# Kernel optimization log

Measured on AMD Instinct MI355X. Metric: run time of the kernel, lower is better.

Reference implementation:

```python
import jax, jax.numpy as jnp
import numpy as np

T = 16384
D_IN = 512
D_HID = 512
D_OUT = 512


def setup_inputs() -> dict:
    key = jax.random.key(0)
    ks = jax.random.split(key, 7)
    s_in = 1.0 / np.sqrt(D_IN)
    s_hid = 1.0 / np.sqrt(D_HID)
    xs = jax.random.normal(ks[0], (T, D_IN), dtype=jnp.float32)
    Wz = jax.random.uniform(ks[1], (D_HID, D_IN), jnp.float32, -s_in, s_in)
    bz = jax.random.uniform(ks[2], (D_HID,), jnp.float32, -s_in, s_in)
    Wh = jax.random.uniform(ks[3], (D_HID, D_IN), jnp.float32, -s_in, s_in)
    bh = jax.random.uniform(ks[4], (D_HID,), jnp.float32, -s_in, s_in)
    Wo = jax.random.uniform(ks[5], (D_OUT, D_HID), jnp.float32, -s_hid, s_hid)
    bo = jax.random.uniform(ks[6], (D_OUT,), jnp.float32, -s_hid, s_hid)
    return {"xs": xs, "Wz": Wz, "bz": bz, "Wh": Wh, "bh": bh, "Wo": Wo, "bo": bo}


def _combine(first, second):
    a0, b0 = first
    a1, b1 = second
    return (a0 * a1, a1 * b0 + b1)


def reference(xs, Wz, bz, Wh, bh, Wo, bo):
    # gates and candidate hidden states: [T, H]
    zs = jax.nn.sigmoid(xs @ Wz.T + bz)
    hs = xs @ Wh.T + bh
    # prepend identity element (a=1, b=0) for the h_0 = 0 initial state
    a = jnp.concatenate([jnp.ones((1, zs.shape[1]), zs.dtype), 1.0 - zs], axis=0)
    b = jnp.concatenate([jnp.zeros((1, zs.shape[1]), zs.dtype), zs * hs], axis=0)
    _, states = jax.lax.associative_scan(_combine, (a, b))  # [T+1, H]
    return states[1:] @ Wo.T + bo  # [T, D_OUT]
```

## Files before the change

kernel.cpp:

```cpp
#include <hip/hip_runtime.h>
#include <hip/hip_bf16.h>
#include <cstdint>
#include <cmath>

#define T_SEQ 16384
#define DMODEL 512
#define NCHUNK 512
#define LCHUNK 32
#define XS_N   (T_SEQ * DMODEL)
#define W_N    (DMODEL * DMODEL)
#define N4_XS  (XS_N / 4)
#define N4_W   (W_N / 4)
#define N4_TOT (N4_XS + 3 * N4_W)

typedef __bf16 bf16x8 __attribute__((ext_vector_type(8)));
typedef float  f32x4  __attribute__((ext_vector_type(4)));

using bf16 = __hip_bfloat16;

__device__ __forceinline__ void load_lds16(const void* g, void* l) {
    __builtin_amdgcn_global_load_lds((const __attribute__((address_space(1))) void*)g,
                                     (__attribute__((address_space(3))) void*)l,
                                     16, 0, 0);
}

__device__ __forceinline__ unsigned short f2bf(float f) {
    union { float f; unsigned u; } v; v.f = f;
    const unsigned r = (v.u + 0x7FFFu + ((v.u >> 16) & 1u)) >> 16;
    return (unsigned short)r;
}
__device__ __forceinline__ float bf2f(unsigned short u) {
    union { unsigned u; float f; } v; v.u = ((unsigned)u) << 16;
    return v.f;
}

__global__ __launch_bounds__(256) void k_convert(
    const float* __restrict__ xs, const float* __restrict__ Wz,
    const float* __restrict__ Wh, const float* __restrict__ Wo,
    bf16* __restrict__ xs_c, bf16* __restrict__ Wz_c,
    bf16* __restrict__ Wh_c, bf16* __restrict__ Wo_c)
{
    const int i = blockIdx.x * 256 + threadIdx.x;
    if (i >= N4_TOT) return;
    const float* src;
    bf16* dst;
    int o;
    if (i < N4_XS) { src = xs; dst = xs_c; o = i; }
    else {
        const int j = i - N4_XS;
        const int w = j >> 16;
        o = j & 65535;
        src = (w == 0) ? Wz : (w == 1) ? Wh : Wo;
        dst = (w == 0) ? Wz_c : (w == 1) ? Wh_c : Wo_c;
    }
    const float4 v = ((const float4*)src)[o];
    ushort4 r;
    r.x = f2bf(v.x); r.y = f2bf(v.y); r.z = f2bf(v.z); r.w = f2bf(v.w);
    ((ushort4*)dst)[o] = r;
}

__global__ __launch_bounds__(256, 2) void gemm_zh(
    const bf16* __restrict__ xs, const bf16* __restrict__ Wz, const float* __restrict__ bz,
    const bf16* __restrict__ Wh, const float* __restrict__ bh,
    unsigned int* __restrict__ ab_ws)
{
    __shared__ __bf16 As[128 * 64];
    __shared__ __bf16 Zs[128 * 64];
    __shared__ __bf16 Hs[128 * 64];

    const int tid  = threadIdx.x;
    const int bn   = blockIdx.x;
    const int bm   = blockIdx.y;
    const int lane = tid & 63;
    const int wave = tid >> 6;
    const int wm   = wave >> 1;
    const int wn   = wave & 1;

    f32x4 accz[4][4], acch[4][4];
    #pragma unroll
    for (int i = 0; i < 4; ++i)
        #pragma unroll
        for (int j = 0; j < 4; ++j) {
            accz[i][j] = (f32x4){0.f, 0.f, 0.f, 0.f};
            acch[i][j] = (f32x4){0.f, 0.f, 0.f, 0.f};
        }

    const int row0 = tid >> 3;
    const int k8   = tid & 7;

    const bf16* xg = xs + (size_t)(bm * 128) * DMODEL + k8 * 8;
    const bf16* zg = Wz + (size_t)(bn * 128) * DMODEL + k8 * 8;
    const bf16* hg = Wh + (size_t)(bn * 128) * DMODEL + k8 * 8;

    const int quad = lane >> 4;
    const int col  = lane & 15;

    for (int k0 = 0; k0 < DMODEL; k0 += 64) {
        #pragma unroll
        for (int it = 0; it < 4; ++it) {
            const int row   = row0 + it * 32;
            const int chunk = it * 256 + tid;
            load_lds16(xg + (size_t)row * DMODEL + k0, &As[chunk * 8]);
            load_lds16(zg + (size_t)row * DMODEL + k0, &Zs[chunk * 8]);
            load_lds16(hg + (size_t)row * DMODEL + k0, &Hs[chunk * 8]);
        }
        __syncthreads();

        #pragma unroll
        for (int kk = 0; kk < 2; ++kk) {
            const int kb = kk * 32 + quad * 8;
            bf16x8 af[4], zf[4], hf[4];
            #pragma unroll
            for (int i = 0; i < 4; ++i) {
                const int am  = wm * 64 + i * 16 + col;
                const int bnr = wn * 64 + i * 16 + col;
                af[i] = *(const bf16x8*)&As[am * 64 + kb];
                zf[i] = *(const bf16x8*)&Zs[bnr * 64 + kb];
                hf[i] = *(const bf16x8*)&Hs[bnr * 64 + kb];
            }
            #pragma unroll
            for (int i = 0; i < 4; ++i)
                #pragma unroll
                for (int j = 0; j < 4; ++j) {
                    accz[i][j] = __builtin_amdgcn_mfma_f32_16x16x32_bf16(af[i], zf[j], accz[i][j], 0, 0, 0);
                    acch[i][j] = __builtin_amdgcn_mfma_f32_16x16x32_bf16(af[i], hf[j], acch[i][j], 0, 0, 0);
                }
        }
        __syncthreads();
    }

    #pragma unroll
    for (int j = 0; j < 4; ++j) {
        const int n = bn * 128 + wn * 64 + j * 16 + col;
        const float bzv = bz[n];
        const float bhv = bh[n];
        #pragma unroll
        for (int i = 0; i < 4; ++i) {
            const int mbase = bm * 128 + wm * 64 + i * 16 + quad * 4;
            #pragma unroll
            for (int r = 0; r < 4; ++r) {
                const float zpre = accz[i][j][r] + bzv;
                const float hpre = acch[i][j][r] + bhv;
                const float z = 1.f / (1.f + __expf(-zpre));
                const float a = 1.f - z;
                const float b = z * hpre;
                const size_t idx = (size_t)(mbase + r) * DMODEL + n;
                ab_ws[idx] = (unsigned)f2bf(a) | ((unsigned)f2bf(b) << 16);
            }
        }
    }
}

__global__ __launch_bounds__(512) void scan_phase1(
    const unsigned int* __restrict__ ab_ws,
    float* __restrict__ Aagg, float* __restrict__ Bagg)
{
    const int h = threadIdx.x;
    const int c = blockIdx.x;
    const int t0 = c * LCHUNK;
    float A = 1.f, B = 0.f;
    #pragma unroll 8
    for (int i = 0; i < LCHUNK; ++i) {
        const unsigned u = ab_ws[(size_t)(t0 + i) * DMODEL + h];
        const float a = bf2f((unsigned short)(u & 0xFFFFu));
        const float b = bf2f((unsigned short)(u >> 16));
        A = a * A;
        B = a * B + b;
    }
    Aagg[(size_t)c * DMODEL + h] = A;
    Bagg[(size_t)c * DMODEL + h] = B;
}

__global__ __launch_bounds__(NCHUNK) void scan_phase2(
    const float* __restrict__ Aagg, const float* __restrict__ Bagg,
    float* __restrict__ Hpre)
{
    const int h = blockIdx.x;
    const int c = threadIdx.x;
    __shared__ float sA[NCHUNK], sB[NCHUNK];

    float A = Aagg[(size_t)c * DMODEL + h];
    float B = Bagg[(size_t)c * DMODEL + h];
    sA[c] = A; sB[c] = B;
    __syncthreads();

    for (int off = 1; off < NCHUNK; off <<= 1) {
        float pA = 1.f, pB = 0.f;
        if (c >= off) { pA = sA[c - off]; pB = sB[c - off]; }
        __syncthreads();
        const float nA = A * pA;
        const float nB = A * pB + B;
        A = nA; B = nB;
        sA[c] = A; sB[c] = B;
        __syncthreads();
    }
    const float hpre = (c == 0) ? 0.f : sB[c - 1];
    Hpre[(size_t)c * DMODEL + h] = hpre;
}

__global__ __launch_bounds__(512) void scan_phase3(
    const unsigned int* __restrict__ ab_ws,
    const float* __restrict__ Hpre, bf16* __restrict__ states)
{
    const int h = threadIdx.x;
    const int c = blockIdx.x;
    const int t0 = c * LCHUNK;
    float H = Hpre[(size_t)c * DMODEL + h];
    #pragma unroll 8
    for (int i = 0; i < LCHUNK; ++i) {
        const size_t idx = (size_t)(t0 + i) * DMODEL + h;
        const unsigned u = ab_ws[idx];
        const float a = bf2f((unsigned short)(u & 0xFFFFu));
        const float b = bf2f((unsigned short)(u >> 16));
        H = a * H + b;
        ((unsigned short*)states)[idx] = f2bf(H);
    }
}

__global__ __launch_bounds__(256, 2) void gemm_out(
    const bf16* __restrict__ states, const bf16* __restrict__ Wo, const float* __restrict__ bo,
    float* __restrict__ out)
{
    __shared__ __bf16 As[128 * 64];
    __shared__ __bf16 Bs[128 * 64];

    const int tid  = threadIdx.x;
    const int bn   = blockIdx.x;
    const int bm   = blockIdx.y;
    const int lane = tid & 63;
    const int wave = tid >> 6;
    const int wm   = wave >> 1;
    const int wn   = wave & 1;

    f32x4 acc[4][4];
    #pragma unroll
    for (int i = 0; i < 4; ++i)
        #pragma unroll
        for (int j = 0; j < 4; ++j)
            acc[i][j] = (f32x4){0.f, 0.f, 0.f, 0.f};

    const int row0 = tid >> 3;
    const int k8   = tid & 7;

    const bf16* ag = states + (size_t)(bm * 128) * DMODEL + k8 * 8;
    const bf16* bg = Wo     + (size_t)(bn * 128) * DMODEL + k8 * 8;

    const int quad = lane >> 4;
    const int col  = lane & 15;

    for (int k0 = 0; k0 < DMODEL; k0 += 64) {
        #pragma unroll
        for (int it = 0; it < 4; ++it) {
            const int row   = row0 + it * 32;
            const int chunk = it * 256 + tid;
            load_lds16(ag + (size_t)row * DMODEL + k0, &As[chunk * 8]);
            load_lds16(bg + (size_t)row * DMODEL + k0, &Bs[chunk * 8]);
        }
        __syncthreads();

        #pragma unroll
        for (int kk = 0; kk < 2; ++kk) {
            const int kb = kk * 32 + quad * 8;
            bf16x8 af[4], bf[4];
            #pragma unroll
            for (int i = 0; i < 4; ++i) {
                af[i] = *(const bf16x8*)&As[(wm * 64 + i * 16 + col) * 64 + kb];
                bf[i] = *(const bf16x8*)&Bs[(wn * 64 + i * 16 + col) * 64 + kb];
            }
            #pragma unroll
            for (int i = 0; i < 4; ++i)
                #pragma unroll
                for (int j = 0; j < 4; ++j)
                    acc[i][j] = __builtin_amdgcn_mfma_f32_16x16x32_bf16(af[i], bf[j], acc[i][j], 0, 0, 0);
        }
        __syncthreads();
    }

    #pragma unroll
    for (int j = 0; j < 4; ++j) {
        const int n = bn * 128 + wn * 64 + j * 16 + col;
        const float bov = bo[n];
        #pragma unroll
        for (int i = 0; i < 4; ++i) {
            const int mbase = bm * 128 + wm * 64 + i * 16 + quad * 4;
            #pragma unroll
            for (int r = 0; r < 4; ++r)
                out[(size_t)(mbase + r) * DMODEL + n] = acc[i][j][r] + bov;
        }
    }
}

extern "C" void kernel_launch(void* const* d_in, const int* in_sizes, int n_in,
                              void* d_out, int out_size, void* d_ws, size_t ws_size,
                              hipStream_t stream)
{
    const float* xs = (const float*)d_in[0];
    const float* Wz = (const float*)d_in[1];
    const float* bz = (const float*)d_in[2];
    const float* Wh = (const float*)d_in[3];
    const float* bh = (const float*)d_in[4];
    const float* Wo = (const float*)d_in[5];
    const float* bo = (const float*)d_in[6];
    float* out = (float*)d_out;

    char* w = (char*)d_ws;
    bf16*  xs_c   = (bf16*) (w);
    bf16*  Wz_c   = (bf16*) (w + 16777216ull);
    bf16*  Wh_c   = (bf16*) (w + 17301504ull);
    bf16*  Wo_c   = (bf16*) (w + 17825792ull);
    unsigned int* ab_ws = (unsigned int*)(w + 18350080ull);
    bf16*  states = (bf16*) (w + 51904512ull);
    float* Aagg   = (float*)(w + 68681728ull);
    float* Bagg   = (float*)(w + 69730304ull);
    float* Hpre   = (float*)(w + 70778880ull);

    k_convert<<<(N4_TOT + 255) / 256, 256, 0, stream>>>(xs, Wz, Wh, Wo, xs_c, Wz_c, Wh_c, Wo_c);
    gemm_zh<<<dim3(4, 128), 256, 0, stream>>>(xs_c, Wz_c, bz, Wh_c, bh, ab_ws);
    scan_phase1<<<NCHUNK, 512, 0, stream>>>(ab_ws, Aagg, Bagg);
    scan_phase2<<<DMODEL, NCHUNK, 0, stream>>>(Aagg, Bagg, Hpre);
    scan_phase3<<<NCHUNK, 512, 0, stream>>>(ab_ws, Hpre, states);
    gemm_out<<<dim3(4, 128), 256, 0, stream>>>(states, Wo_c, bo, out);
}
```

Measured before the change: 160.2 us.

## Fuse three scan phases into one cooperative kernel with grid syncs

Merges the three scan kernels into a single cooperative launch that uses grid-wide synchronization between the chunk-aggregate, cross-chunk prefix, and chunk-apply phases. If the cooperative launch fails, it falls back to the original three launches. The aim is to remove two kernel launch gaps and their tail drain. In exchange, grid.sync has its own cost and the 512 blocks of 512 threads must all be co-resident.

Result: slower. 288.1 us (+79.8%).

```diff
diff --git a/kernel.cpp b/kernel.cpp
--- a/kernel.cpp
+++ b/kernel.cpp
@@ -1,7 +1,10 @@
 #include <hip/hip_runtime.h>
 #include <hip/hip_bf16.h>
+#include <hip/hip_cooperative_groups.h>
 #include <cstdint>
 #include <cmath>
+
+namespace cg = cooperative_groups;
 
 #define T_SEQ 16384
 #define DMODEL 512
@@ -151,17 +154,15 @@
     }
 }
 
-__global__ __launch_bounds__(512) void scan_phase1(
+__device__ __forceinline__ void phase1_body(
     const unsigned int* __restrict__ ab_ws,
-    float* __restrict__ Aagg, float* __restrict__ Bagg)
-{
-    const int h = threadIdx.x;
-    const int c = blockIdx.x;
-    const int t0 = c * LCHUNK;
+    float* __restrict__ Aagg, float* __restrict__ Bagg, int c, int h)
+{
+    const size_t base = (size_t)(c * LCHUNK) * DMODEL + h;
     float A = 1.f, B = 0.f;
     #pragma unroll 8
     for (int i = 0; i < LCHUNK; ++i) {
-        const unsigned u = ab_ws[(size_t)(t0 + i) * DMODEL + h];
+        const unsigned u = ab_ws[base + (size_t)i * DMODEL];
         const float a = bf2f((unsigned short)(u & 0xFFFFu));
         const float b = bf2f((unsigned short)(u >> 16));
         A = a * A;
@@ -171,51 +172,76 @@
     Bagg[(size_t)c * DMODEL + h] = B;
 }
 
-__global__ __launch_bounds__(NCHUNK) void scan_phase2(
+__device__ __forceinline__ void phase2_body(
     const float* __restrict__ Aagg, const float* __restrict__ Bagg,
-    float* __restrict__ Hpre)
-{
-    const int h = blockIdx.x;
-    const int c = threadIdx.x;
-    __shared__ float sA[NCHUNK], sB[NCHUNK];
-
+    float* __restrict__ Hpre, float* sA, float* sB, int h, int c)
+{
     float A = Aagg[(size_t)c * DMODEL + h];
     float B = Bagg[(size_t)c * DMODEL + h];
     sA[c] = A; sB[c] = B;
     __syncthreads();
-
     for (int off = 1; off < NCHUNK; off <<= 1) {
         float pA = 1.f, pB = 0.f;
         if (c >= off) { pA = sA[c - off]; pB = sB[c - off]; }
         __syncthreads();
+        const float nB = A * pB + B;
         const float nA = A * pA;
-        const float nB = A * pB + B;
         A = nA; B = nB;
         sA[c] = A; sB[c] = B;
         __syncthreads();
     }
-    const float hpre = (c == 0) ? 0.f : sB[c - 1];
-    Hpre[(size_t)c * DMODEL + h] = hpre;
-}
-
-__global__ __launch_bounds__(512) void scan_phase3(
-    const unsigned int* __restrict__ ab_ws,
-    const float* __restrict__ Hpre, bf16* __restrict__ states)
-{
-    const int h = threadIdx.x;
-    const int c = blockIdx.x;
-    const int t0 = c * LCHUNK;
+    const float hp = (c == 0) ? 0.f : sB[c - 1];
+    Hpre[(size_t)c * DMODEL + h] = hp;
+}
+
+__device__ __forceinline__ void phase3_body(
+    const unsigned int* __restrict__ ab_ws, const float* __restrict__ Hpre,
+    unsigned short* __restrict__ states, int c, int h)
+{
     float H = Hpre[(size_t)c * DMODEL + h];
+    const size_t base = (size_t)(c * LCHUNK) * DMODEL + h;
     #pragma unroll 8
     for (int i = 0; i < LCHUNK; ++i) {
-        const size_t idx = (size_t)(t0 + i) * DMODEL + h;
-        const unsigned u = ab_ws[idx];
+        const unsigned u = ab_ws[base + (size_t)i * DMODEL];
         const float a = bf2f((unsigned short)(u & 0xFFFFu));
         const float b = bf2f((unsigned short)(u >> 16));
         H = a * H + b;
-        ((unsigned short*)states)[idx] = f2bf(H);
-    }
-}
+        states[base + (size_t)i * DMODEL] = f2bf(H);
+    }
+}
+
+__global__ __launch_bounds__(512, 4) void scan_fused(
+    const unsigned int* __restrict__ ab_ws,
+    float* __restrict__ Aagg, float* __restrict__ Bagg,
+    float* __restrict__ Hpre, unsigned short* __restrict__ states)
+{
+    cg::grid_group grid = cg::this_grid();
+    __shared__ float sA[NCHUNK], sB[NCHUNK];
+    const int tid = threadIdx.x;
+    const int blk = blockIdx.x;
+
+    phase1_body(ab_ws, Aagg, Bagg, blk, tid);
+    grid.sync();
+    phase2_body(Aagg, Bagg, Hpre, sA, sB, blk, tid);
+    grid.sync();
+    phase3_body(ab_ws, Hpre, states, blk, tid);
+}
+
+__global__ __launch_bounds__(512) void scan_p1(
+    const unsigned int* __restrict__ ab_ws, float* __restrict__ Aagg, float* __restrict__ Bagg)
+{ phase1_body(ab_ws, Aagg, Bagg, blockIdx.x, threadIdx.x); }
+
+__global__ __launch_bounds__(512) void scan_p2(
+    const float* __restrict__ Aagg, const float* __restrict__ Bagg, float* __restrict__ Hpre)
+{
+    __shared__ float sA[NCHUNK], sB[NCHUNK];
+    phase2_body(Aagg, Bagg, Hpre, sA, sB, blockIdx.x, threadIdx.x);
+}
+
+__global__ __launch_bounds__(512) void scan_p3(
+    const unsigned int* __restrict__ ab_ws, const float* __restrict__ Hpre,
+    unsigned short* __restrict__ states)
+{ phase3_body(ab_ws, Hpre, states, blockIdx.x, threadIdx.x); }
 
 __global__ __launch_bounds__(256, 2) void gemm_out(
     const bf16* __restrict__ states, const bf16* __restrict__ Wo, const float* __restrict__ bo,
@@ -308,16 +334,23 @@
     bf16*  Wz_c   = (bf16*) (w + 16777216ull);
     bf16*  Wh_c   = (bf16*) (w + 17301504ull);
     bf16*  Wo_c   = (bf16*) (w + 17825792ull);
-    unsigned int* ab_ws = (unsigned int*)(w + 18350080ull);
-    bf16*  states = (bf16*) (w + 51904512ull);
+    unsigned int*   ab_ws  = (unsigned int*)  (w + 18350080ull);
+    unsigned short* states = (unsigned short*)(w + 51904512ull);
     float* Aagg   = (float*)(w + 68681728ull);
     float* Bagg   = (float*)(w + 69730304ull);
     float* Hpre   = (float*)(w + 70778880ull);
 
     k_convert<<<(N4_TOT + 255) / 256, 256, 0, stream>>>(xs, Wz, Wh, Wo, xs_c, Wz_c, Wh_c, Wo_c);
     gemm_zh<<<dim3(4, 128), 256, 0, stream>>>(xs_c, Wz_c, bz, Wh_c, bh, ab_ws);
-    scan_phase1<<<NCHUNK, 512, 0, stream>>>(ab_ws, Aagg, Bagg);
-    scan_phase2<<<DMODEL, NCHUNK, 0, stream>>>(Aagg, Bagg, Hpre);
-    scan_phase3<<<NCHUNK, 512, 0, stream>>>(ab_ws, Hpre, states);
-    gemm_out<<<dim3(4, 128), 256, 0, stream>>>(states, Wo_c, bo, out);
-}
+
+    void* args[] = { (void*)&ab_ws, (void*)&Aagg, (void*)&Bagg, (void*)&Hpre, (void*)&states };
+    hipError_t ce = hipLaunchCooperativeKernel((void*)scan_fused, dim3(NCHUNK), dim3(512),
+                                               args, 0, stream);
+    if (ce != hipSuccess) {
+        scan_p1<<<NCHUNK, 512, 0, stream>>>(ab_ws, Aagg, Bagg);
+        scan_p2<<<DMODEL, 512, 0, stream>>>(Aagg, Bagg, Hpre);
+        scan_p3<<<NCHUNK, 512, 0, stream>>>(ab_ws, Hpre, states);
+    }
+
+    gemm_out<<<dim3(4, 128), 256, 0, stream>>>((const bf16*)states, Wo_c, bo, out);
+}
```

## Fuse scan phase-1 chunk aggregation into gate GEMM epilogue via wave shuffles

Applied to the files above, without the earlier changes.

The gate/candidate GEMM epilogue now computes per-chunk (A,B) scan aggregates directly from its accumulators. It combines across quads with xor-shuffles and writes Aagg/Bagg, which removes the separate scan_phase1 kernel and its full re-read of the ab workspace. The scan_phase3 kernel is rewritten with 256 threads processing two columns each using 64-bit vector loads and stores. The GEMM grids are transposed so blockIdx.x walks the M dimension, which changes block scheduling order and L2 reuse of weights. Aggregates are computed from fp32 values rather than the bf16-rounded ones, so they differ slightly from what phase 3 replays.

New measurement: 152.3 us. -4.9%, faster.

```diff
diff --git a/kernel.cpp b/kernel.cpp
--- a/kernel.cpp
+++ b/kernel.cpp
@@ -32,6 +32,12 @@
 __device__ __forceinline__ float bf2f(unsigned short u) {
     union { unsigned u; float f; } v; v.u = ((unsigned)u) << 16;
     return v.f;
+}
+
+__device__ __forceinline__ void comb(float& A, float& B, float fA, float fB,
+                                     float sA, float sB) {
+    A = fA * sA;
+    B = sA * fB + sB;
 }
 
 __global__ __launch_bounds__(256) void k_convert(
@@ -62,15 +68,16 @@
 __global__ __launch_bounds__(256, 2) void gemm_zh(
     const bf16* __restrict__ xs, const bf16* __restrict__ Wz, const float* __restrict__ bz,
     const bf16* __restrict__ Wh, const float* __restrict__ bh,
-    unsigned int* __restrict__ ab_ws)
+    unsigned int* __restrict__ ab_ws,
+    float* __restrict__ Aagg, float* __restrict__ Bagg)
 {
     __shared__ __bf16 As[128 * 64];
     __shared__ __bf16 Zs[128 * 64];
     __shared__ __bf16 Hs[128 * 64];
 
     const int tid  = threadIdx.x;
-    const int bn   = blockIdx.x;
-    const int bm   = blockIdx.y;
+    const int bm   = blockIdx.x;
+    const int bn   = blockIdx.y;
     const int lane = tid & 63;
     const int wave = tid >> 6;
     const int wm   = wave >> 1;
@@ -129,14 +136,17 @@
         __syncthreads();
     }
 
+    const int c_lo = bm * 4 + wm * 2;
     #pragma unroll
     for (int j = 0; j < 4; ++j) {
         const int n = bn * 128 + wn * 64 + j * 16 + col;
         const float bzv = bz[n];
         const float bhv = bh[n];
+        float cA[4], cB[4];
         #pragma unroll
         for (int i = 0; i < 4; ++i) {
             const int mbase = bm * 128 + wm * 64 + i * 16 + quad * 4;
+            float A = 1.f, B = 0.f;
             #pragma unroll
             for (int r = 0; r < 4; ++r) {
                 const float zpre = accz[i][j][r] + bzv;
@@ -146,32 +156,37 @@
                 const float b = z * hpre;
                 const size_t idx = (size_t)(mbase + r) * DMODEL + n;
                 ab_ws[idx] = (unsigned)f2bf(a) | ((unsigned)f2bf(b) << 16);
+                A = a * A;
+                B = a * B + b;
             }
-        }
-    }
-}
-
-__global__ __launch_bounds__(512) void scan_phase1(
-    const unsigned int* __restrict__ ab_ws,
-    float* __restrict__ Aagg, float* __restrict__ Bagg)
-{
-    const int h = threadIdx.x;
-    const int c = blockIdx.x;
-    const int t0 = c * LCHUNK;
-    float A = 1.f, B = 0.f;
-    #pragma unroll 8
-    for (int i = 0; i < LCHUNK; ++i) {
-        const unsigned u = ab_ws[(size_t)(t0 + i) * DMODEL + h];
-        const float a = bf2f((unsigned short)(u & 0xFFFFu));
-        const float b = bf2f((unsigned short)(u >> 16));
-        A = a * A;
-        B = a * B + b;
-    }
-    Aagg[(size_t)c * DMODEL + h] = A;
-    Bagg[(size_t)c * DMODEL + h] = B;
-}
-
-__global__ __launch_bounds__(NCHUNK) void scan_phase2(
+            cA[i] = A; cB[i] = B;
+        }
+        #pragma unroll
+        for (int i = 0; i < 4; ++i) {
+            float pA = __shfl_xor(cA[i], 16);
+            float pB = __shfl_xor(cB[i], 16);
+            const bool hi1 = quad & 1;
+            comb(cA[i], cB[i], hi1 ? pA : cA[i], hi1 ? pB : cB[i],
+                               hi1 ? cA[i] : pA, hi1 ? cB[i] : pB);
+            pA = __shfl_xor(cA[i], 32);
+            pB = __shfl_xor(cB[i], 32);
+            const bool hi2 = quad >> 1;
+            comb(cA[i], cB[i], hi2 ? pA : cA[i], hi2 ? pB : cB[i],
+                               hi2 ? cA[i] : pA, hi2 ? cB[i] : pB);
+        }
+        float Alo, Blo, Ahi, Bhi;
+        comb(Alo, Blo, cA[0], cB[0], cA[1], cB[1]);
+        comb(Ahi, Bhi, cA[2], cB[2], cA[3], cB[3]);
+        if (quad == 0) {
+            Aagg[(size_t)c_lo * DMODEL + n]       = Alo;
+            Bagg[(size_t)c_lo * DMODEL + n]       = Blo;
+            Aagg[(size_t)(c_lo + 1) * DMODEL + n] = Ahi;
+            Bagg[(size_t)(c_lo + 1) * DMODEL + n] = Bhi;
+        }
+    }
+}
+
+__global__ __launch_bounds__(512) void scan_p2(
     const float* __restrict__ Aagg, const float* __restrict__ Bagg,
     float* __restrict__ Hpre)
 {
@@ -188,32 +203,37 @@
         float pA = 1.f, pB = 0.f;
         if (c >= off) { pA = sA[c - off]; pB = sB[c - off]; }
         __syncthreads();
+        const float nB = A * pB + B;
         const float nA = A * pA;
-        const float nB = A * pB + B;
         A = nA; B = nB;
         sA[c] = A; sB[c] = B;
         __syncthreads();
     }
-    const float hpre = (c == 0) ? 0.f : sB[c - 1];
-    Hpre[(size_t)c * DMODEL + h] = hpre;
-}
-
-__global__ __launch_bounds__(512) void scan_phase3(
-    const unsigned int* __restrict__ ab_ws,
-    const float* __restrict__ Hpre, bf16* __restrict__ states)
-{
-    const int h = threadIdx.x;
-    const int c = blockIdx.x;
-    const int t0 = c * LCHUNK;
-    float H = Hpre[(size_t)c * DMODEL + h];
+    const float hp = (c == 0) ? 0.f : sB[c - 1];
+    Hpre[(size_t)c * DMODEL + h] = hp;
+}
+
+__global__ __launch_bounds__(256) void scan_p3(
+    const unsigned int* __restrict__ ab_ws, const float* __restrict__ Hpre,
+    unsigned short* __restrict__ states)
+{
+    const int tid = threadIdx.x;
+    const int c   = blockIdx.x;
+    const float2 hp = ((const float2*)(Hpre + (size_t)c * DMODEL))[tid];
+    float H0 = hp.x, H1 = hp.y;
+    const size_t rowbase = (size_t)(c * LCHUNK) * DMODEL;
     #pragma unroll 8
     for (int i = 0; i < LCHUNK; ++i) {
-        const size_t idx = (size_t)(t0 + i) * DMODEL + h;
-        const unsigned u = ab_ws[idx];
-        const float a = bf2f((unsigned short)(u & 0xFFFFu));
-        const float b = bf2f((unsigned short)(u >> 16));
-        H = a * H + b;
-        ((unsigned short*)states)[idx] = f2bf(H);
+        const size_t row = rowbase + (size_t)i * DMODEL;
+        const uint2 u = ((const uint2*)(ab_ws + row))[tid];
+        const float a0 = bf2f((unsigned short)(u.x & 0xFFFFu));
+        const float b0 = bf2f((unsigned short)(u.x >> 16));
+        const float a1 = bf2f((unsigned short)(u.y & 0xFFFFu));
+        const float b1 = bf2f((unsigned short)(u.y >> 16));
+        H0 = a0 * H0 + b0;
+        H1 = a1 * H1 + b1;
+        ushort2 s; s.x = f2bf(H0); s.y = f2bf(H1);
+        ((ushort2*)(states + row))[tid] = s;
     }
 }
 
@@ -225,8 +245,8 @@
     __shared__ __bf16 Bs[128 * 64];
 
     const int tid  = threadIdx.x;
-    const int bn   = blockIdx.x;
-    const int bm   = blockIdx.y;
+    const int bm   = blockIdx.x;
+    const int bn   = blockIdx.y;
     const int lane = tid & 63;
     const int wave = tid >> 6;
     const int wm   = wave >> 1;
@@ -308,16 +328,15 @@
     bf16*  Wz_c   = (bf16*) (w + 16777216ull);
     bf16*  Wh_c   = (bf16*) (w + 17301504ull);
     bf16*  Wo_c   = (bf16*) (w + 17825792ull);
-    unsigned int* ab_ws = (unsigned int*)(w + 18350080ull);
-    bf16*  states = (bf16*) (w + 51904512ull);
+    unsigned int*   ab_ws  = (unsigned int*)  (w + 18350080ull);
+    unsigned short* states = (unsigned short*)(w + 51904512ull);
     float* Aagg   = (float*)(w + 68681728ull);
     float* Bagg   = (float*)(w + 69730304ull);
     float* Hpre   = (float*)(w + 70778880ull);
 
     k_convert<<<(N4_TOT + 255) / 256, 256, 0, stream>>>(xs, Wz, Wh, Wo, xs_c, Wz_c, Wh_c, Wo_c);
-    gemm_zh<<<dim3(4, 128), 256, 0, stream>>>(xs_c, Wz_c, bz, Wh_c, bh, ab_ws);
-    scan_phase1<<<NCHUNK, 512, 0, stream>>>(ab_ws, Aagg, Bagg);
-    scan_phase2<<<DMODEL, NCHUNK, 0, stream>>>(Aagg, Bagg, Hpre);
-    scan_phase3<<<NCHUNK, 512, 0, stream>>>(ab_ws, Hpre, states);
-    gemm_out<<<dim3(4, 128), 256, 0, stream>>>(states, Wo_c, bo, out);
-}
+    gemm_zh<<<dim3(128, 4), 256, 0, stream>>>(xs_c, Wz_c, bz, Wh_c, bh, ab_ws, Aagg, Bagg);
+    scan_p2<<<DMODEL, NCHUNK, 0, stream>>>(Aagg, Bagg, Hpre);
+    scan_p3<<<NCHUNK, 256, 0, stream>>>(ab_ws, Hpre, states);
+    gemm_out<<<dim3(128, 4), 256, 0, stream>>>((const bf16*)states, Wo_c, bo, out);
+}
```
